# Performance work log

Hardware: AMD Instinct MI355X
Metric: run time of the kernel (lower is better)

## Reference

```python
import jax, jax.numpy as jnp
import numpy as np

CH, XH, YH, RADIUS = 2, 2, 2, 1  # channel_heads, x_heads, y_heads, neighborhood radius


def neighborhood_mask(n_sub_x, n_sub_y, radius):
    # clamped neighbor offsets reduce to |di|<=r and |dj|<=r within the grid
    iy = jnp.arange(n_sub_y)
    ix = jnp.arange(n_sub_x)
    my = jnp.abs(iy[:, None] - iy[None, :]) <= radius  # [ny, ny]
    mx = jnp.abs(ix[:, None] - ix[None, :]) <= radius  # [nx, nx]
    m = my[:, None, :, None] & mx[None, :, None, :]    # [ny, nx, ny, nx]
    s = n_sub_x * n_sub_y
    return m.reshape(s, s)  # row-major (h1 w1)(h2 w2), matching einops


def setup_inputs() -> dict:
    key = jax.random.key(0)
    k1, k2, k3 = jax.random.split(key, 3)
    C = 128
    seq = jax.random.normal(k1, (2, 256, C, 16, 16), dtype=jnp.float32)
    w_qkv = jax.random.normal(k2, (3 * C, C), dtype=jnp.float32) / np.sqrt(C).astype(np.float32)
    w_out = jax.random.normal(k3, (C, C), dtype=jnp.float32) / np.sqrt(C).astype(np.float32)
    b_out = jnp.zeros((C,), dtype=jnp.float32)
    return {"seq": seq, "w_qkv": w_qkv, "w_out": w_out, "b_out": b_out,
            "n_sub_x": 16, "n_sub_y": 16}


def reference(seq, w_qkv, w_out, b_out, n_sub_x, n_sub_y):
    b, s, C, H, W = seq.shape
    h, w = H // YH, W // XH
    c = C // CH
    nH = YH * XH * CH  # total heads

    # pointwise qkv projection over channels: [b, s, 3C, H, W]
    qkv = jnp.einsum('bschw,dc->bsdhw', seq, w_qkv)

    # decompose2d: split spatial grid into y_heads x x_heads blocks -> spatial heads
    # [b, s, 3C, YH, h, XH, w] -> [b, s, YH*XH, 3C, h, w]
    qkv = qkv.reshape(b, s, 3 * C, YH, h, XH, w)
    qkv = qkv.transpose(0, 1, 3, 5, 2, 4, 6).reshape(b, s, YH * XH, 3 * C, h, w)

    # split into q,k,v and channel heads: 3C = 3 * CH * c
    qkv = qkv.reshape(b, s, YH * XH, 3, CH, c, h, w)
    # -> [3, b, (spatial_heads * channel_heads), s, c, h, w]
    qkv = qkv.transpose(3, 0, 2, 4, 1, 5, 6, 7).reshape(3, b, nH, s, c, h, w)
    q, k, v = qkv[0], qkv[1], qkv[2]

    # scaled dot-product attention over flattened function dim (c,h,w)
    scale = 1.0 / np.sqrt(c * h * w).astype(np.float32)
    scores = jnp.einsum('bnschw,bntchw->bnst', q, k) * scale  # [b, nH, s, s]
    mask = neighborhood_mask(n_sub_x, n_sub_y, RADIUS)  # [s, s]
    scores = jnp.where(mask[None, None, :, :], scores, jnp.finfo(scores.dtype).min)
    attn = jax.nn.softmax(scores, axis=-1)
    sa = jnp.einsum('bnst,bntchw->bnschw', attn, v)  # [b, nH, s, c, h, w]

    # merge channel heads back: [b, s, spatial_heads, C, h, w]
    sa = sa.reshape(b, YH * XH, CH, s, c, h, w)
    sa = sa.transpose(0, 3, 1, 2, 4, 5, 6).reshape(b, s, YH, XH, C, h, w)
    # recompose2d: [b, s, C, H, W]
    sa = sa.transpose(0, 1, 4, 2, 5, 3, 6).reshape(b, s, C, H, W)

    # output pointwise projection with bias
    out = jnp.einsum('bschw,dc->bsdhw', sa, w_out) + b_out[None, None, :, None, None]
    return out
```

## Files before the change

### kernel.cpp

```cpp
#include <hip/hip_runtime.h>

#define BATCH 2
#define SS    256
#define CC    128
#define HWN   256
#define FDIM  4096

typedef unsigned int uint;
typedef unsigned short ushort;
typedef short bf16x8 __attribute__((ext_vector_type(8)));
typedef ushort us4 __attribute__((ext_vector_type(4)));
typedef float f32x4 __attribute__((ext_vector_type(4)));

__device__ __forceinline__ ushort f2b(float f) {
  uint u = __float_as_uint(f);
  return (ushort)((u + 0x7fffu + ((u >> 16) & 1u)) >> 16);
}
__device__ __forceinline__ float b2f(ushort h) { return __uint_as_float((uint)h << 16); }

__global__ __launch_bounds__(512, 4) void k_qkv(const float* __restrict__ seq,
                                                const float* __restrict__ wqkv,
                                                ushort* __restrict__ qkvh) {
  __shared__ ushort wlds[128 * 128];
  const int bs = blockIdx.x;
  const int b = bs >> 8, s = bs & 255;
  const int t = threadIdx.x;
  const int wv = t >> 6, lane = t & 63;
  const int qq = lane >> 4, m = lane & 15;

  const float* sp = seq + (size_t)bs * (CC * HWN);

  bf16x8 bfrag[2][4];
  uint obase[2];
  #pragma unroll
  for (int set = 0; set < 2; ++set) {
    const int ntg = wv * 2 + set;
    const int hw = ntg * 16 + m;
    #pragma unroll
    for (int ks = 0; ks < 4; ++ks) {
      const int k0 = ks * 32 + qq * 8;
      float tmp[8];
      #pragma unroll
      for (int j = 0; j < 8; ++j) tmp[j] = sp[(k0 + j) * HWN + hw];
      bf16x8 fr;
      #pragma unroll
      for (int j = 0; j < 8; ++j) fr[j] = (short)f2b(tmp[j]);
      bfrag[set][ks] = fr;
    }
    const int n_qk = ((ntg >> 3) * 2 + (m >> 3)) * 2;
    const int hwl  = (ntg & 7) * 8 + (m & 7);
    obase[set] = (uint)(((b * 8 + n_qk) * SS + s) * FDIM + hwl * 16 + qq * 4);
  }

  for (int qkvi = 0; qkvi < 3; ++qkvi) {
    if (qkvi) __syncthreads();
    #pragma unroll
    for (int i = 0; i < 4; ++i) {
      const int row = i * 32 + (t >> 4), col16 = t & 15;
      const float* wp = wqkv + (size_t)(qkvi * 128 + row) * 128 + col16 * 8;
      f32x4 w0 = *(const f32x4*)(wp);
      f32x4 w1 = *(const f32x4*)(wp + 4);
      bf16x8 fr;
      #pragma unroll
      for (int e = 0; e < 4; ++e) { fr[e] = (short)f2b(w0[e]); fr[4 + e] = (short)f2b(w1[e]); }
      *(bf16x8*)&wlds[row * 128 + ((col16 ^ (row & 15)) * 8)] = fr;
    }
    __syncthreads();

    #pragma unroll
    for (int mt8 = 0; mt8 < 8; ++mt8) {
      bf16x8 afrag[4];
      #pragma unroll
      for (int ks = 0; ks < 4; ++ks)
        afrag[ks] = *(const bf16x8*)&wlds[(mt8 * 16 + m) * 128 + (((ks * 4 + qq) ^ m) * 8)];
      const int ch = mt8 >> 2, m4 = mt8 & 3;
      #pragma unroll
      for (int set = 0; set < 2; ++set) {
        f32x4 acc = {0.f, 0.f, 0.f, 0.f};
        #pragma unroll
        for (int ks = 0; ks < 4; ++ks)
          acc = __builtin_amdgcn_mfma_f32_16x16x32_bf16(afrag[ks], bfrag[set][ks], acc, 0, 0, 0);
        us4 pk;
        #pragma unroll
        for (int r = 0; r < 4; ++r) pk[r] = f2b(acc[r]);
        *(us4*)(qkvh + obase[set]
                + (uint)((qkvi * 16 + ch) * (SS * FDIM) + m4 * 1024)) = pk;
      }
    }
  }
}

__global__ __launch_bounds__(1024) void k_scores(const ushort* __restrict__ qkvh,
                                                 float* __restrict__ attn) {
  __shared__ float red[16][64][12];
  const int g = blockIdx.x;
  const int unit = (g & 7) * 32 + (g >> 3);
  const int b  = unit >> 7;
  const int n  = (unit >> 4) & 7;
  const int sy = unit & 15;
  const int t = threadIdx.x;
  const int wave = t >> 6, lane = t & 63;
  const int qq = lane >> 4, l15 = lane & 15;
  const size_t hs = (size_t)SS * FDIM;
  const ushort* qb = qkvh + (size_t)(b * 8 + n) * hs;
  const ushort* kb = qkvh + (size_t)(16 + b * 8 + n) * hs;

  const ushort* qp = qb + (size_t)(sy * 16 + l15) * FDIM + qq * 8;
  const ushort* kp[3];
  #pragma unroll
  for (int tl = 0; tl < 3; ++tl) {
    const int tyc = min(max(sy - 1 + tl, 0), 15);
    kp[tl] = kb + (size_t)(tyc * 16 + l15) * FDIM + qq * 8;
  }

  f32x4 acc[3] = {{0,0,0,0},{0,0,0,0},{0,0,0,0}};
  const int kbeg = wave * 256;
  #pragma unroll
  for (int it = 0; it < 4; ++it) {
    const int k0 = kbeg + it * 64;
    bf16x8 a0 = *(const bf16x8*)(qp + k0);
    bf16x8 a1 = *(const bf16x8*)(qp + k0 + 32);
    bf16x8 b0[3], b1[3];
    #pragma unroll
    for (int tl = 0; tl < 3; ++tl) {
      b0[tl] = *(const bf16x8*)(kp[tl] + k0);
      b1[tl] = *(const bf16x8*)(kp[tl] + k0 + 32);
    }
    #pragma unroll
    for (int tl = 0; tl < 3; ++tl)
      acc[tl] = __builtin_amdgcn_mfma_f32_16x16x32_bf16(a0, b0[tl], acc[tl], 0, 0, 0);
    #pragma unroll
    for (int tl = 0; tl < 3; ++tl)
      acc[tl] = __builtin_amdgcn_mfma_f32_16x16x32_bf16(a1, b1[tl], acc[tl], 0, 0, 0);
  }

  #pragma unroll
  for (int tl = 0; tl < 3; ++tl)
    #pragma unroll
    for (int r = 0; r < 4; ++r) red[wave][lane][tl * 4 + r] = acc[tl][r];
  __syncthreads();
  if (t < 768) {
    const int lane2 = t / 12, idx = t - lane2 * 12;
    float ssum = red[0][lane2][idx];
    #pragma unroll
    for (int w = 1; w < 16; ++w) ssum += red[w][lane2][idx];
    red[0][lane2][idx] = ssum;
  }
  __syncthreads();
  if (wave != 0) return;
  #pragma unroll
  for (int tl = 0; tl < 3; ++tl)
    #pragma unroll
    for (int r = 0; r < 4; ++r) acc[tl][r] = red[0][lane][tl * 4 + r];

  const int tx = l15;
  float sc[3][4];
  #pragma unroll
  for (int tl = 0; tl < 3; ++tl) {
    const int ty = sy - 1 + tl;
    const bool tyv = (ty >= 0 && ty < 16);
    #pragma unroll
    for (int r = 0; r < 4; ++r) {
      const int sx = qq * 4 + r;
      const bool v = tyv && (tx - sx <= 1) && (sx - tx <= 1);
      sc[tl][r] = v ? acc[tl][r] * (1.f / 64.f) : -1e30f;
    }
  }
  #pragma unroll
  for (int r = 0; r < 4; ++r) {
    float mx = fmaxf(fmaxf(sc[0][r], sc[1][r]), sc[2][r]);
    #pragma unroll
    for (int off = 1; off < 16; off <<= 1) mx = fmaxf(mx, __shfl_xor(mx, off));
    float p[3], sum = 0.f;
    #pragma unroll
    for (int tl = 0; tl < 3; ++tl) { p[tl] = __expf(sc[tl][r] - mx); sum += p[tl]; }
    #pragma unroll
    for (int off = 1; off < 16; off <<= 1) sum += __shfl_xor(sum, off);
    const float inv = 1.f / sum;
    const int sx = qq * 4 + r;
    const int s = sy * 16 + sx;
    #pragma unroll
    for (int tl = 0; tl < 3; ++tl) {
      const int ty = sy - 1 + tl;
      const int dxp = tx - sx + 1;
      if (ty >= 0 && ty < 16 && dxp >= 0 && dxp <= 2)
        attn[((size_t)(b * 8 + n) * SS + s) * 9 + tl * 3 + dxp] = p[tl] * inv;
    }
  }
}

__global__ __launch_bounds__(256) void k_pv(const ushort* __restrict__ qkvh,
                                            const float* __restrict__ attn,
                                            ushort* __restrict__ sa) {
  const int g = blockIdx.x;
  const int unit = (g & 7) * 512 + (g >> 3);
  const int eta = unit >> 8, s = unit & 255;
  const int sy = s >> 4, sx = s & 15;
  const int t = threadIdx.x;
  const size_t hs = (size_t)SS * FDIM;

  float p[9];
  int sjc[9];
  bool vld[9];
  #pragma unroll
  for (int j = 0; j < 9; ++j) {
    const int ny = sy + j / 3 - 1, nx = sx + j % 3 - 1;
    vld[j] = (ny >= 0 && ny < 16 && nx >= 0 && nx < 16);
    sjc[j] = min(max(ny, 0), 15) * 16 + min(max(nx, 0), 15);
    p[j] = vld[j] ? attn[((size_t)eta * SS + s) * 9 + j] : 0.f;
  }

  const ushort* vb = qkvh + (size_t)(32 + eta) * hs;
  const int f0 = t * 16;
  float acc[16];
  #pragma unroll
  for (int e = 0; e < 16; ++e) acc[e] = 0.f;
  #pragma unroll
  for (int j = 0; j < 9; ++j) {
    if (vld[j]) {
      const ushort* vp = vb + (size_t)sjc[j] * FDIM + f0;
      bf16x8 v0 = *(const bf16x8*)(vp);
      bf16x8 v1 = *(const bf16x8*)(vp + 8);
      const float pj = p[j];
      #pragma unroll
      for (int e = 0; e < 8; ++e) acc[e]     += pj * b2f((ushort)v0[e]);
      #pragma unroll
      for (int e = 0; e < 8; ++e) acc[8 + e] += pj * b2f((ushort)v1[e]);
    }
  }
  bf16x8 r0, r1;
  #pragma unroll
  for (int e = 0; e < 8; ++e) { r0[e] = (short)f2b(acc[e]); r1[e] = (short)f2b(acc[8 + e]); }
  ushort* op = sa + ((size_t)eta * SS + s) * FDIM + f0;
  *(bf16x8*)op = r0;
  *(bf16x8*)(op + 8) = r1;
}

__global__ __launch_bounds__(256) void k_proj(const ushort* __restrict__ qkvh,
                                              const float* __restrict__ wout,
                                              const float* __restrict__ bout,
                                              float* __restrict__ out) {
  __shared__ ushort wlds[128 * 128];
  const int g = blockIdx.x;
  const int r9 = g >> 3;
  const int G = (g & 7) * 4 + (r9 >> 6);
  const int idx = r9 & 63;
  const int b = G >> 4, sy = G & 15;
  const int sx = idx >> 2, sub = idx & 3;
  const int s = sy * 16 + sx;
  const int bs = b * 256 + s;
  const int t = threadIdx.x;
  const int wave = t >> 6, lane = t & 63;
  const int ntg = sub * 4 + wave;
  const int qq = lane >> 4, m = lane & 15;
  const size_t hs = (size_t)SS * FDIM;

  {
    const int col16 = t & 15;
    const int ks = col16 >> 2, qw = col16 & 3;
    const int creal0 = (ks >> 1) * 64 + ((((ks & 1) << 1) | (qw >> 1)) << 4)
                       + ((qw & 1) << 3);
    #pragma unroll
    for (int i = 0; i < 8; ++i) {
      const int row = i * 16 + (t >> 4);
      const float* wp = wout + (size_t)row * 128 + creal0;
      f32x4 w0 = *(const f32x4*)(wp);
      f32x4 w1 = *(const f32x4*)(wp + 4);
      bf16x8 fr;
      #pragma unroll
      for (int e = 0; e < 4; ++e) { fr[e] = (short)f2b(w0[e]); fr[4 + e] = (short)f2b(w1[e]); }
      *(bf16x8*)&wlds[row * 128 + ((col16 ^ (row & 15)) * 8)] = fr;
    }
  }

  const int nbase = ((ntg >> 3) * 2 + (m >> 3)) * 2;
  const int hwl = (ntg & 7) * 8 + (m & 7);
  bf16x8 bfrag[4];
  #pragma unroll
  for (int ks = 0; ks < 4; ++ks) {
    const int ch = ks >> 1;
    const int c64hi = ((ks & 1) << 1) | (qq >> 1);
    const int half = qq & 1;
    const ushort* sb = qkvh + (size_t)(b * 8 + nbase + ch) * hs;
    const int off = c64hi * 1024 + hwl * 16 + half * 8;
    bfrag[ks] = *(const bf16x8*)(sb + (size_t)s * FDIM + off);
  }

  __syncthreads();

  #pragma unroll
  for (int mt = 0; mt < 8; ++mt) {
    bf16x8 afrag[4];
    #pragma unroll
    for (int ks = 0; ks < 4; ++ks)
      afrag[ks] = *(const bf16x8*)&wlds[(mt * 16 + m) * 128 + (((ks * 4 + qq) ^ m) * 8)];
    f32x4 acc = {0.f, 0.f, 0.f, 0.f};
    #pragma unroll
    for (int ks = 0; ks < 4; ++ks)
      acc = __builtin_amdgcn_mfma_f32_16x16x32_bf16(afrag[ks], bfrag[ks], acc, 0, 0, 0);
    const int hw = ntg * 16 + m;
    #pragma unroll
    for (int r = 0; r < 4; ++r) {
      const int d = mt * 16 + qq * 4 + r;
      out[((size_t)bs * CC + d) * HWN + hw] = acc[r] + bout[d];
    }
  }
}

extern "C" void kernel_launch(void* const* d_in, const int* in_sizes, int n_in,
                              void* d_out, int out_size, void* d_ws, size_t ws_size,
                              hipStream_t stream) {
  const float* seq  = (const float*)d_in[0];
  const float* wqkv = (const float*)d_in[1];
  const float* wout = (const float*)d_in[2];
  const float* bout = (const float*)d_in[3];
  char* ws = (char*)d_ws;
  ushort* qkvh = (ushort*)(ws);
  float*  attn = (float*)(ws + 100663296ull);
  float*  outp = (float*)d_out;

  hipLaunchKernelGGL(k_qkv,    dim3(512),  dim3(512),  0, stream, seq, wqkv, qkvh);
  hipLaunchKernelGGL(k_scores, dim3(256),  dim3(1024), 0, stream, qkvh, attn);
  hipLaunchKernelGGL(k_pv,     dim3(4096), dim3(256),  0, stream, qkvh, attn, qkvh );
  hipLaunchKernelGGL(k_proj,   dim3(2048), dim3(256),  0, stream, qkvh, wout, bout, outp);
}
```

Baseline: 195.2 us.

## Fuse attention-weighted V aggregation into output projection kernel

```diff
diff --git a/kernel.cpp b/kernel.cpp
--- a/kernel.cpp
+++ b/kernel.cpp
@@ -189,57 +189,11 @@
   }
 }
 
-__global__ __launch_bounds__(256) void k_pv(const ushort* __restrict__ qkvh,
-                                            const float* __restrict__ attn,
-                                            ushort* __restrict__ sa) {
-  const int g = blockIdx.x;
-  const int unit = (g & 7) * 512 + (g >> 3);
-  const int eta = unit >> 8, s = unit & 255;
-  const int sy = s >> 4, sx = s & 15;
-  const int t = threadIdx.x;
-  const size_t hs = (size_t)SS * FDIM;
-
-  float p[9];
-  int sjc[9];
-  bool vld[9];
-  #pragma unroll
-  for (int j = 0; j < 9; ++j) {
-    const int ny = sy + j / 3 - 1, nx = sx + j % 3 - 1;
-    vld[j] = (ny >= 0 && ny < 16 && nx >= 0 && nx < 16);
-    sjc[j] = min(max(ny, 0), 15) * 16 + min(max(nx, 0), 15);
-    p[j] = vld[j] ? attn[((size_t)eta * SS + s) * 9 + j] : 0.f;
-  }
-
-  const ushort* vb = qkvh + (size_t)(32 + eta) * hs;
-  const int f0 = t * 16;
-  float acc[16];
-  #pragma unroll
-  for (int e = 0; e < 16; ++e) acc[e] = 0.f;
-  #pragma unroll
-  for (int j = 0; j < 9; ++j) {
-    if (vld[j]) {
-      const ushort* vp = vb + (size_t)sjc[j] * FDIM + f0;
-      bf16x8 v0 = *(const bf16x8*)(vp);
-      bf16x8 v1 = *(const bf16x8*)(vp + 8);
-      const float pj = p[j];
-      #pragma unroll
-      for (int e = 0; e < 8; ++e) acc[e]     += pj * b2f((ushort)v0[e]);
-      #pragma unroll
-      for (int e = 0; e < 8; ++e) acc[8 + e] += pj * b2f((ushort)v1[e]);
-    }
-  }
-  bf16x8 r0, r1;
-  #pragma unroll
-  for (int e = 0; e < 8; ++e) { r0[e] = (short)f2b(acc[e]); r1[e] = (short)f2b(acc[8 + e]); }
-  ushort* op = sa + ((size_t)eta * SS + s) * FDIM + f0;
-  *(bf16x8*)op = r0;
-  *(bf16x8*)(op + 8) = r1;
-}
-
-__global__ __launch_bounds__(256) void k_proj(const ushort* __restrict__ qkvh,
-                                              const float* __restrict__ wout,
-                                              const float* __restrict__ bout,
-                                              float* __restrict__ out) {
+__global__ __launch_bounds__(256) void k_out(const ushort* __restrict__ qkvh,
+                                             const float* __restrict__ attn,
+                                             const float* __restrict__ wout,
+                                             const float* __restrict__ bout,
+                                             float* __restrict__ out) {
   __shared__ ushort wlds[128 * 128];
   const int g = blockIdx.x;
   const int r9 = g >> 3;
@@ -273,7 +227,26 @@
     }
   }
 
+  int sjc[9];
+  bool vld[9];
+  #pragma unroll
+  for (int j = 0; j < 9; ++j) {
+    const int ny = sy + j / 3 - 1, nx = sx + j % 3 - 1;
+    vld[j] = (ny >= 0 && ny < 16 && nx >= 0 && nx < 16);
+    sjc[j] = min(max(ny, 0), 15) * 16 + min(max(nx, 0), 15);
+  }
+
   const int nbase = ((ntg >> 3) * 2 + (m >> 3)) * 2;
+  float pch[2][9];
+  #pragma unroll
+  for (int ch = 0; ch < 2; ++ch) {
+    #pragma unroll
+    for (int j = 0; j < 9; ++j) {
+      const float w = attn[((size_t)(b * 8 + nbase + ch) * SS + s) * 9 + j];
+      pch[ch][j] = vld[j] ? w : 0.f;
+    }
+  }
+
   const int hwl = (ntg & 7) * 8 + (m & 7);
   bf16x8 bfrag[4];
   #pragma unroll
@@ -281,9 +254,20 @@
     const int ch = ks >> 1;
     const int c64hi = ((ks & 1) << 1) | (qq >> 1);
     const int half = qq & 1;
-    const ushort* sb = qkvh + (size_t)(b * 8 + nbase + ch) * hs;
+    const ushort* vb = qkvh + (size_t)(32 + b * 8 + nbase + ch) * hs;
     const int off = c64hi * 1024 + hwl * 16 + half * 8;
-    bfrag[ks] = *(const bf16x8*)(sb + (size_t)s * FDIM + off);
+    float facc[8] = {0.f, 0.f, 0.f, 0.f, 0.f, 0.f, 0.f, 0.f};
+    #pragma unroll
+    for (int j = 0; j < 9; ++j) {
+      bf16x8 vv = *(const bf16x8*)(vb + (size_t)sjc[j] * FDIM + off);
+      const float pj = pch[ch][j];
+      #pragma unroll
+      for (int e = 0; e < 8; ++e) facc[e] += pj * b2f((ushort)vv[e]);
+    }
+    bf16x8 fr;
+    #pragma unroll
+    for (int e = 0; e < 8; ++e) fr[e] = (short)f2b(facc[e]);
+    bfrag[ks] = fr;
   }
 
   __syncthreads();
@@ -321,6 +305,5 @@
 
   hipLaunchKernelGGL(k_qkv,    dim3(512),  dim3(512),  0, stream, seq, wqkv, qkvh);
   hipLaunchKernelGGL(k_scores, dim3(256),  dim3(1024), 0, stream, qkvh, attn);
-  hipLaunchKernelGGL(k_pv,     dim3(4096), dim3(256),  0, stream, qkvh, attn, qkvh );
-  hipLaunchKernelGGL(k_proj,   dim3(2048), dim3(256),  0, stream, qkvh, wout, bout, outp);
-}
+  hipLaunchKernelGGL(k_out,    dim3(2048), dim3(256),  0, stream, qkvh, attn, wout, bout, outp);
+}
```

Measured after the change: 188.4 us. 1.04x faster.
